# Kernel optimization log

Measured on AMD Instinct MI355X. Metric: run time of the kernel, lower is better.

## Reference

```python
import jax, jax.numpy as jnp
import numpy as np
from jax import lax

# Model dims (mamba_ssm defaults: d_state=16, d_conv=4, expand=2, dt_rank=ceil(d_model/16))
V = 16384       # vocab_size
D = 1024        # embedding_dim / d_model
C_CLS = 128     # num_CLS_classes
D_INNER = 2 * D # expand * d_model = 2048
N = 16          # d_state
K = 4           # d_conv
DT_RANK = (D + 15) // 16  # 64
B, L = 4, 512


def setup_inputs() -> dict:
    key = jax.random.key(0)
    ks = jax.random.split(key, 12)
    s = 0.02
    tokens = jax.random.randint(ks[0], (B, L), 0, V, dtype=jnp.int64)
    embedding = jax.random.normal(ks[1], (V, D), jnp.float32) * s
    in_proj_w = jax.random.normal(ks[2], (2 * D_INNER, D), jnp.float32) * s
    conv_w = jax.random.normal(ks[3], (D_INNER, 1, K), jnp.float32) * 0.1
    conv_b = jnp.zeros((D_INNER,), jnp.float32)
    x_proj_w = jax.random.normal(ks[4], (DT_RANK + 2 * N, D_INNER), jnp.float32) * s
    dt_proj_w = jax.random.normal(ks[5], (D_INNER, DT_RANK), jnp.float32) * s
    dt_proj_b = jax.random.uniform(ks[6], (D_INNER,), jnp.float32, -4.0, -2.0)  # softplus -> small dt
    A_log = jnp.log(jnp.broadcast_to(jnp.arange(1, N + 1, dtype=jnp.float32), (D_INNER, N)))
    D_param = jnp.ones((D_INNER,), jnp.float32)
    out_proj_w = jax.random.normal(ks[7], (D, D_INNER), jnp.float32) * s
    recon_w = jax.random.normal(ks[8], (V, D), jnp.float32) * s
    cls_w = jax.random.normal(ks[9], (C_CLS, D), jnp.float32) * s
    return dict(tokens=tokens, embedding=embedding, in_proj_w=in_proj_w,
                conv_w=conv_w, conv_b=conv_b, x_proj_w=x_proj_w,
                dt_proj_w=dt_proj_w, dt_proj_b=dt_proj_b, A_log=A_log,
                D_param=D_param, out_proj_w=out_proj_w, recon_w=recon_w, cls_w=cls_w)


def _mamba(h, in_proj_w, conv_w, conv_b, x_proj_w, dt_proj_w, dt_proj_b, A_log, D_param, out_proj_w):
    # h: (B, L, D)
    xz = jnp.einsum('bld,ed->ble', h, in_proj_w)          # (B, L, 2*D_INNER)
    x, z = jnp.split(xz, 2, axis=-1)                      # each (B, L, D_INNER)
    # causal depthwise conv1d along L
    xt = jnp.swapaxes(x, 1, 2)                            # (B, D_INNER, L)
    xt = lax.conv_general_dilated(xt, conv_w, window_strides=(1,),
                                  padding=[(K - 1, 0)],
                                  feature_group_count=D_INNER,
                                  dimension_numbers=('NCH', 'OIH', 'NCH'))
    xt = xt + conv_b[None, :, None]
    x = jax.nn.silu(jnp.swapaxes(xt, 1, 2))               # (B, L, D_INNER)
    # input-dependent dt, B, C
    x_dbl = jnp.einsum('bld,ed->ble', x, x_proj_w)        # (B, L, DT_RANK+2N)
    dt, Bm, Cm = jnp.split(x_dbl, [DT_RANK, DT_RANK + N], axis=-1)
    delta = jax.nn.softplus(jnp.einsum('blr,dr->bld', dt, dt_proj_w) + dt_proj_b)  # (B,L,D_INNER)
    A = -jnp.exp(A_log)                                   # (D_INNER, N)
    dA = jnp.exp(delta[..., None] * A)                    # (B,L,D_INNER,N)
    dBx = delta[..., None] * Bm[:, :, None, :] * x[..., None]  # (B,L,D_INNER,N)
    # selective scan over time (sequential recurrence)
    dA_t = jnp.swapaxes(dA, 0, 1)                         # (L,B,D_INNER,N)
    dBx_t = jnp.swapaxes(dBx, 0, 1)
    C_t = jnp.swapaxes(Cm, 0, 1)                          # (L,B,N)
    def step(hc, inp):
        a, bx, c = inp
        hc = a * hc + bx                                  # (B,D_INNER,N)
        y = jnp.einsum('bdn,bn->bd', hc, c)
        return hc, y
    h0 = jnp.zeros((x.shape[0], D_INNER, N), x.dtype)
    _, ys = lax.scan(step, h0, (dA_t, dBx_t, C_t))
    y = jnp.swapaxes(ys, 0, 1) + x * D_param              # (B,L,D_INNER)
    y = y * jax.nn.silu(z)
    return jnp.einsum('ble,de->bld', y, out_proj_w)       # (B,L,D)


def reference(tokens, embedding, in_proj_w, conv_w, conv_b, x_proj_w,
              dt_proj_w, dt_proj_b, A_log, D_param, out_proj_w, recon_w, cls_w):
    h = embedding[tokens]                                 # (B,L,D)
    h = _mamba(h, in_proj_w, conv_w, conv_b, x_proj_w, dt_proj_w, dt_proj_b,
               A_log, D_param, out_proj_w)
    recon = jnp.einsum('bld,vd->blv', h, recon_w)         # (B,L,V)
    pooled = h.mean(axis=1)                               # mean CLS pooling assumption
    cls = jnp.einsum('bd,cd->bc', pooled, cls_w)          # (B,C_CLS)
    return (recon, cls)
```

## Files before the change

### kernel.cpp

```cpp
#include <hip/hip_runtime.h>
#include <hip/hip_bf16.h>
#include <stdint.h>

#define DIN    2048
#define MROWS  2048
#define LSEQ   512
#define NV     16384
#define DMODEL 1024
#define NC     8
#define CL     64

typedef __attribute__((ext_vector_type(8))) short bf16x8;
typedef __attribute__((ext_vector_type(4))) float f32x4;

__device__ __forceinline__ uint16_t f2bf(float f) {
  uint32_t u = __builtin_bit_cast(uint32_t, f);
  u += 0x7fffu + ((u >> 16) & 1u);
  return (uint16_t)(u >> 16);
}
__device__ __forceinline__ float bf2f(uint16_t u) {
  return __builtin_bit_cast(float, (uint32_t)u << 16);
}

__device__ __forceinline__ void gld_lds16(const uint16_t* g, uint16_t* l) {
  __builtin_amdgcn_global_load_lds(
      (const __attribute__((address_space(1))) void*)g,
      (__attribute__((address_space(3))) void*)l,
      16, 0, 0);
}

__global__ __launch_bounds__(512, 2) void gemm256_bf16_kernel(
    const uint16_t* __restrict__ A, const uint16_t* __restrict__ B,
    float* __restrict__ C, int M, int N, int K)
{
  __shared__ uint16_t lds[4 * 16384];
  const int tid = threadIdx.x;
  const int w   = tid >> 6;
  const int l   = tid & 63;

  const int nwg = gridDim.x;
  const int cpx = nwg >> 3;
  const int swz = (blockIdx.x & 7) * cpx + (blockIdx.x >> 3);
  const int nmy = M >> 8;
  const int bm  = (swz % nmy) << 8;
  const int bn  = (swz / nmy) << 8;

  const int fr = l & 15;
  const int fg = l >> 4;
  const int wr = w >> 2;
  const int wc = w & 3;

  const int srow = l >> 2;
  const int kof  = (((l & 3) ^ ((l >> 3) & 3)) << 3);
  const int ar0  = (w * 2 + 0) * 16 + srow;
  const int ar1  = (w * 2 + 1) * 16 + srow;
  const uint16_t* Ag0 = A + (size_t)(bm + ar0) * K + kof;
  const uint16_t* Ag1 = A + (size_t)(bm + ar1) * K + kof;
  const uint16_t* Bg0 = B + (size_t)(bn + ar0) * K + kof;
  const uint16_t* Bg1 = B + (size_t)(bn + ar1) * K + kof;
  const int lA0 = (w * 2 + 0) * 512;
  const int lA1 = (w * 2 + 1) * 512;
  const int lB0 = 8192 + (w * 2 + 0) * 512;
  const int lB1 = 8192 + (w * 2 + 1) * 512;

  const int axr  = ((fg ^ ((fr >> 1) & 3)) << 3);
  const int aoff = (wr * 128 + fr) * 32 + axr;
  const int boff = 8192 + (wc * 64 + fr) * 32 + axr;

  f32x4 acc[8][4] = {};
  const int NT = K >> 5;

  auto stage = [&](int t) {
    const int sb = (t & 3) << 14;
    const int k0 = t << 5;
    gld_lds16(Ag0 + k0, lds + sb + lA0);
    gld_lds16(Ag1 + k0, lds + sb + lA1);
    gld_lds16(Bg0 + k0, lds + sb + lB0);
    gld_lds16(Bg1 + k0, lds + sb + lB1);
  };
  auto compute_tile = [&](int sb) {
    bf16x8 af[8], bfr[4];
#pragma unroll
    for (int mi = 0; mi < 8; ++mi)
      af[mi] = *(const bf16x8*)(lds + sb + aoff + mi * 512);
#pragma unroll
    for (int ni = 0; ni < 4; ++ni)
      bfr[ni] = *(const bf16x8*)(lds + sb + boff + ni * 512);
    __builtin_amdgcn_s_setprio(1);
#pragma unroll
    for (int mi = 0; mi < 8; ++mi)
#pragma unroll
      for (int ni = 0; ni < 4; ++ni)
        acc[mi][ni] = __builtin_amdgcn_mfma_f32_16x16x32_bf16(af[mi], bfr[ni], acc[mi][ni], 0, 0, 0);
    __builtin_amdgcn_s_setprio(0);
  };

  stage(0); stage(1); stage(2);
  asm volatile("s_waitcnt vmcnt(8)" ::: "memory");
  __builtin_amdgcn_s_barrier();

  for (int t = 0; t < NT - 3; ++t) {
    stage(t + 3);
    compute_tile((t & 3) << 14);
    asm volatile("s_waitcnt vmcnt(8)" ::: "memory");
    __builtin_amdgcn_s_barrier();
  }
  compute_tile(((NT - 3) & 3) << 14);
  asm volatile("s_waitcnt vmcnt(4)" ::: "memory");
  __builtin_amdgcn_s_barrier();
  compute_tile(((NT - 2) & 3) << 14);
  asm volatile("s_waitcnt vmcnt(0)" ::: "memory");
  __builtin_amdgcn_s_barrier();
  compute_tile(((NT - 1) & 3) << 14);

#pragma unroll
  for (int mi = 0; mi < 8; ++mi) {
    const int r0 = bm + wr * 128 + mi * 16 + fg * 4;
#pragma unroll
    for (int ni = 0; ni < 4; ++ni) {
      const int c0 = bn + wc * 64 + ni * 16 + fr;
#pragma unroll
      for (int r = 0; r < 4; ++r)
        C[(size_t)(r0 + r) * N + c0] = acc[mi][ni][r];
    }
  }
}

__global__ __launch_bounds__(256) void gemm_bf16_kernel(
    const uint16_t* __restrict__ A, const uint16_t* __restrict__ B,
    float* __restrict__ C, int M, int N, int K, int kchunk,
    const float* __restrict__ bias)
{
  __shared__ uint16_t As[128 * 32];
  __shared__ uint16_t Bs[128 * 32];
  const int tid  = threadIdx.x;
  const int wid  = tid >> 6;
  const int lane = tid & 63;
  const int bm = blockIdx.y * 128;
  const int bn = blockIdx.x * 128;
  const int k_beg = blockIdx.z * kchunk;
  float* Cout = C + (size_t)blockIdx.z * M * N;

  const int fr = lane & 15;
  const int fg = lane >> 4;
  const int wm = (wid >> 1) * 64;
  const int wn = (wid & 1) * 64;

  const int srow = wid * 32 + (lane >> 2);
  const int skof = (((lane & 3) ^ ((lane >> 2) & 3)) << 3);
  const uint16_t* Ag = A + (size_t)(bm + srow) * K + skof;
  const uint16_t* Bg = B + (size_t)(bn + srow) * K + skof;
  uint16_t* Al = As + wid * 1024;
  uint16_t* Bl = Bs + wid * 1024;

  const int cxr = ((fg ^ (fr & 3)) << 3);

  f32x4 acc[4][4] = {};

  for (int k0 = 0; k0 < kchunk; k0 += 32) {
    const int kk = k_beg + k0;
    gld_lds16(Ag + kk, Al);
    gld_lds16(Ag + (size_t)16 * K + kk, Al + 512);
    gld_lds16(Bg + kk, Bl);
    gld_lds16(Bg + (size_t)16 * K + kk, Bl + 512);
    asm volatile("s_waitcnt vmcnt(0)" ::: "memory");
    __syncthreads();
    bf16x8 af[4], bfr[4];
#pragma unroll
    for (int i = 0; i < 4; ++i)
      af[i] = *(const bf16x8*)(As + (wm + i * 16 + fr) * 32 + cxr);
#pragma unroll
    for (int j = 0; j < 4; ++j)
      bfr[j] = *(const bf16x8*)(Bs + (wn + j * 16 + fr) * 32 + cxr);
#pragma unroll
    for (int i = 0; i < 4; ++i)
#pragma unroll
      for (int j = 0; j < 4; ++j)
        acc[i][j] = __builtin_amdgcn_mfma_f32_16x16x32_bf16(af[i], bfr[j], acc[i][j], 0, 0, 0);
    __syncthreads();
  }

#pragma unroll
  for (int i = 0; i < 4; ++i) {
    const int r0 = bm + wm + i * 16 + fg * 4;
#pragma unroll
    for (int j = 0; j < 4; ++j) {
      const int c0 = bn + wn + j * 16 + fr;
      const float bv = bias ? bias[c0] : 0.f;
#pragma unroll
      for (int r = 0; r < 4; ++r) {
        float v = acc[i][j][r];
        if (bias) {
          const float u = v + bv;
          v = (u > 20.f) ? u : log1pf(__expf(u));
        }
        Cout[(size_t)(r0 + r) * N + c0] = v;
      }
    }
  }
}

__global__ __launch_bounds__(256) void reduce8_dt_kernel(
    const float* __restrict__ in, float* __restrict__ xdbl, uint16_t* __restrict__ dtb) {
  const int i = blockIdx.x * 256 + threadIdx.x;
  float s = 0.f;
#pragma unroll
  for (int z = 0; z < 8; ++z) s += in[i + (size_t)z * 262144];
  xdbl[i] = s;
  const int c = i & 127;
  if (c < 64) dtb[(i >> 7) * 64 + c] = f2bf(s);
}

__global__ __launch_bounds__(256) void reduce2_bf16_kernel(
    const float* __restrict__ in, uint16_t* __restrict__ outb, int n) {
  const int i = blockIdx.x * 256 + threadIdx.x;
  if (i >= n) return;
  outb[i] = f2bf(in[i] + in[i + (size_t)n]);
}

__global__ __launch_bounds__(256) void embed_kernel(
    const int* __restrict__ tok, const float* __restrict__ emb, uint16_t* __restrict__ out) {
  const int m = blockIdx.x;
  const int t = tok[m];
  const float4 v = ((const float4*)(emb + (size_t)t * DMODEL))[threadIdx.x];
  ((ushort4*)(out + (size_t)m * DMODEL))[threadIdx.x] =
      make_ushort4(f2bf(v.x), f2bf(v.y), f2bf(v.z), f2bf(v.w));
}

__global__ __launch_bounds__(256) void cvt_bf16_kernel(
    const float* __restrict__ in, uint16_t* __restrict__ out, int n4) {
  const int i = blockIdx.x * 256 + threadIdx.x;
  if (i >= n4) return;
  const float4 v = ((const float4*)in)[i];
  ((ushort4*)out)[i] = make_ushort4(f2bf(v.x), f2bf(v.y), f2bf(v.z), f2bf(v.w));
}

__global__ __launch_bounds__(256) void cvt_pad_kernel(
    const float* __restrict__ in, uint16_t* __restrict__ out, int rows_in, int cols4) {
  const int i = blockIdx.x * 256 + threadIdx.x;
  const int r = i / cols4, c = i % cols4;
  ushort4 o = make_ushort4(0, 0, 0, 0);
  if (r < rows_in) {
    const float4 v = ((const float4*)in)[(size_t)r * cols4 + c];
    o = make_ushort4(f2bf(v.x), f2bf(v.y), f2bf(v.z), f2bf(v.w));
  }
  ((ushort4*)out)[i] = o;
}

__global__ __launch_bounds__(256) void conv_silu_kernel(
    const float* __restrict__ xz, const float* __restrict__ cw, const float* __restrict__ cb,
    float* __restrict__ xc, uint16_t* __restrict__ xcb)
{
  const int idx = blockIdx.x * 256 + threadIdx.x;
  const int d = idx & (DIN - 1);
  const int m = idx >> 11;
  const int l = m & (LSEQ - 1);
  float acc = cb[d];
#pragma unroll
  for (int j = 0; j < 4; ++j) {
    const int lj = l - 3 + j;
    if (lj >= 0) acc += cw[d * 4 + j] * xz[(size_t)(m - 3 + j) * 4096 + d];
  }
  const float r = acc / (1.f + __expf(-acc));
  xc[idx] = r;
  xcb[idx] = f2bf(r);
}

__global__ __launch_bounds__(256) void scan_partial_kernel(
    const float* __restrict__ delta, const float* __restrict__ xc,
    const float* __restrict__ xdbl, const float* __restrict__ A_log,
    float* __restrict__ Pb, float* __restrict__ Qb)
{
  const int q = threadIdx.x & 3;
  const int d_idx = threadIdx.x >> 2;
  const int c = blockIdx.x;
  const int d = blockIdx.y * 64 + d_idx;
  const int b = blockIdx.z;
  float Arow[4];
#pragma unroll
  for (int n = 0; n < 4; ++n)
    Arow[n] = -expf(A_log[d * 16 + q * 4 + n]);
  float P[4] = {1.f, 1.f, 1.f, 1.f};
  float Q[4] = {0.f, 0.f, 0.f, 0.f};
  const int l0 = c * CL;
#pragma unroll 4
  for (int li = 0; li < CL; ++li) {
    const int m = b * LSEQ + l0 + li;
    const float de = delta[(size_t)m * DIN + d];
    const float xv = xc[(size_t)m * DIN + d];
    const float dx = de * xv;
    const float4 Bv = *(const float4*)(xdbl + (size_t)m * 128 + 64 + q * 4);
    const float bv[4] = {Bv.x, Bv.y, Bv.z, Bv.w};
#pragma unroll
    for (int n = 0; n < 4; ++n) {
      const float a = __expf(de * Arow[n]);
      P[n] *= a;
      Q[n] = a * Q[n] + dx * bv[n];
    }
  }
  const size_t o = ((size_t)(b * NC + c) * DIN + d) * 16 + q * 4;
  *(float4*)(Pb + o) = make_float4(P[0], P[1], P[2], P[3]);
  *(float4*)(Qb + o) = make_float4(Q[0], Q[1], Q[2], Q[3]);
}

__global__ __launch_bounds__(256) void scan_bounds_kernel(
    const float* __restrict__ Pb, const float* __restrict__ Qb, float* __restrict__ Hi)
{
  const int i = blockIdx.x * 256 + threadIdx.x;
  const int b = i >> 15;
  const int r = i & 32767;
  float h = 0.f;
#pragma unroll
  for (int c = 0; c < NC; ++c) {
    const size_t o = ((size_t)(b * NC + c) << 15) + r;
    Hi[o] = h;
    h = Pb[o] * h + Qb[o];
  }
}

__global__ __launch_bounds__(256) void scan_final_kernel(
    const float* __restrict__ delta, const float* __restrict__ xc,
    const float* __restrict__ xdbl, const float* __restrict__ xz,
    const float* __restrict__ A_log, const float* __restrict__ Dp,
    const float* __restrict__ Hi, uint16_t* __restrict__ yb)
{
  const int q = threadIdx.x & 3;
  const int d_idx = threadIdx.x >> 2;
  const int c = blockIdx.x;
  const int d = blockIdx.y * 64 + d_idx;
  const int b = blockIdx.z;
  float Arow[4];
#pragma unroll
  for (int n = 0; n < 4; ++n)
    Arow[n] = -expf(A_log[d * 16 + q * 4 + n]);
  const float dpd = Dp[d];
  const size_t o = ((size_t)(b * NC + c) * DIN + d) * 16 + q * 4;
  const float4 Hv = *(const float4*)(Hi + o);
  float h[4] = {Hv.x, Hv.y, Hv.z, Hv.w};
  const int l0 = c * CL;
#pragma unroll 2
  for (int li = 0; li < CL; ++li) {
    const int m = b * LSEQ + l0 + li;
    const float de = delta[(size_t)m * DIN + d];
    const float xv = xc[(size_t)m * DIN + d];
    const float dx = de * xv;
    const float4 Bv = *(const float4*)(xdbl + (size_t)m * 128 + 64 + q * 4);
    const float4 Cv = *(const float4*)(xdbl + (size_t)m * 128 + 80 + q * 4);
    const float bv[4] = {Bv.x, Bv.y, Bv.z, Bv.w};
    const float cv[4] = {Cv.x, Cv.y, Cv.z, Cv.w};
    float yp = 0.f;
#pragma unroll
    for (int n = 0; n < 4; ++n) {
      const float a = __expf(de * Arow[n]);
      h[n] = a * h[n] + dx * bv[n];
      yp += h[n] * cv[n];
    }
    yp += __shfl_xor(yp, 1);
    yp += __shfl_xor(yp, 2);
    if (q == 0) {
      const float z = xz[(size_t)m * 4096 + 2048 + d];
      const float sil = z / (1.f + __expf(-z));
      yb[(size_t)m * DIN + d] = f2bf((yp + xv * dpd) * sil);
    }
  }
}

__global__ __launch_bounds__(256) void pool1_kernel(
    const uint16_t* __restrict__ h2b, float* __restrict__ part) {
  const int b = blockIdx.x >> 4, s = blockIdx.x & 15;
  const int c = threadIdx.x * 4;
  const uint16_t* base = h2b + ((size_t)(b * LSEQ + s * 32)) * DMODEL + c;
  float a0 = 0, a1 = 0, a2 = 0, a3 = 0;
  for (int l = 0; l < 32; ++l) {
    const ushort4 v = *(const ushort4*)(base + (size_t)l * DMODEL);
    a0 += bf2f(v.x); a1 += bf2f(v.y); a2 += bf2f(v.z); a3 += bf2f(v.w);
  }
  *(float4*)(part + (size_t)blockIdx.x * DMODEL + c) = make_float4(a0, a1, a2, a3);
}

__global__ __launch_bounds__(256) void pool2_cls_kernel(
    const float* __restrict__ part, const float* __restrict__ w, float* __restrict__ out) {
  __shared__ float pl[DMODEL];
  const int b = blockIdx.x, t = threadIdx.x;
  float4 s = make_float4(0, 0, 0, 0);
  for (int k = 0; k < 16; ++k) {
    const float4 v = *(const float4*)(part + ((size_t)(b * 16 + k)) * DMODEL + t * 4);
    s.x += v.x; s.y += v.y; s.z += v.z; s.w += v.w;
  }
  const float inv = 1.f / (float)LSEQ;
  pl[t * 4 + 0] = s.x * inv; pl[t * 4 + 1] = s.y * inv;
  pl[t * 4 + 2] = s.z * inv; pl[t * 4 + 3] = s.w * inv;
  __syncthreads();
  if (t < 128) {
    const float* wr = w + (size_t)t * DMODEL;
    float acc = 0.f;
    for (int k = 0; k < DMODEL; ++k) acc += pl[k] * wr[k];
    out[b * 128 + t] = acc;
  }
}

extern "C" void kernel_launch(void* const* d_in, const int* in_sizes, int n_in,
                              void* d_out, int out_size, void* d_ws, size_t ws_size,
                              hipStream_t stream) {
  const int*   tokens    = (const int*)d_in[0];
  const float* embedding = (const float*)d_in[1];
  const float* in_proj_w = (const float*)d_in[2];
  const float* conv_w    = (const float*)d_in[3];
  const float* conv_b    = (const float*)d_in[4];
  const float* x_proj_w  = (const float*)d_in[5];
  const float* dt_proj_w = (const float*)d_in[6];
  const float* dt_proj_b = (const float*)d_in[7];
  const float* A_log     = (const float*)d_in[8];
  const float* D_param   = (const float*)d_in[9];
  const float* out_prj_w = (const float*)d_in[10];
  const float* recon_w   = (const float*)d_in[11];
  const float* cls_w     = (const float*)d_in[12];

  char* ws = (char*)d_ws;
  const size_t MB = 1024 * 1024;
  uint16_t* h_bf   = (uint16_t*)(ws + 0);
  uint16_t* w_in   = (uint16_t*)(ws + 4 * MB);
  float*    xz     = (float*)(ws + 12 * MB);
  float*    xc_f   = (float*)(ws + 44 * MB);
  uint16_t* xc_b   = (uint16_t*)(ws + 60 * MB);
  uint16_t* wx_bf  = (uint16_t*)(ws + 68 * MB);
  float*    xdbl   = (float*)(ws + 69 * MB);
  uint16_t* dt_bf  = (uint16_t*)(ws + 70 * MB);
  uint16_t* wdt_bf = (uint16_t*)(ws + 71 * MB);
  float*    delta  = (float*)(ws + 72 * MB);
  uint16_t* y_bf   = (uint16_t*)(ws + 88 * MB);
  uint16_t* h2_bf  = (uint16_t*)(ws + 96 * MB);
  float*    part   = (float*)(ws + 100 * MB);
  uint16_t* wout_bf = h_bf;
  uint16_t* wrec_bf = (uint16_t*)xz;
  float*    kscr    = delta;
  float*    Pbuf    = (float*)(ws + 60 * MB);
  float*    Qbuf    = (float*)(ws + 64 * MB);
  float*    Hinit   = (float*)(ws + 4 * MB);

  const int RECON = MROWS * NV;

  embed_kernel<<<dim3(MROWS), dim3(256), 0, stream>>>(tokens, embedding, h_bf);
  cvt_bf16_kernel<<<dim3(4096), dim3(256), 0, stream>>>(in_proj_w, w_in, 4096 * 1024 / 4);
  gemm_bf16_kernel<<<dim3(32, 16, 1), dim3(256), 0, stream>>>(h_bf, w_in, xz, MROWS, 4096, 1024, 1024, nullptr);
  cvt_bf16_kernel<<<dim3(2048), dim3(256), 0, stream>>>(out_prj_w, wout_bf, 1024 * 2048 / 4);
  cvt_bf16_kernel<<<dim3(128), dim3(256), 0, stream>>>(dt_proj_w, wdt_bf, 2048 * 64 / 4);
  cvt_pad_kernel<<<dim3(256), dim3(256), 0, stream>>>(x_proj_w, wx_bf, 96, 512);
  conv_silu_kernel<<<dim3(16384), dim3(256), 0, stream>>>(xz, conv_w, conv_b, xc_f, xc_b);
  gemm_bf16_kernel<<<dim3(1, 16, 8), dim3(256), 0, stream>>>(xc_b, wx_bf, kscr, MROWS, 128, 2048, 256, nullptr);
  reduce8_dt_kernel<<<dim3(1024), dim3(256), 0, stream>>>(kscr, xdbl, dt_bf);
  gemm_bf16_kernel<<<dim3(16, 16, 1), dim3(256), 0, stream>>>(dt_bf, wdt_bf, delta, MROWS, DIN, 64, 64, dt_proj_b);
  scan_partial_kernel<<<dim3(NC, 32, 4), dim3(256), 0, stream>>>(delta, xc_f, xdbl, A_log, Pbuf, Qbuf);
  scan_bounds_kernel<<<dim3(512), dim3(256), 0, stream>>>(Pbuf, Qbuf, Hinit);
  scan_final_kernel<<<dim3(NC, 32, 4), dim3(256), 0, stream>>>(delta, xc_f, xdbl, xz, A_log, D_param, Hinit, y_bf);
  cvt_bf16_kernel<<<dim3(16384), dim3(256), 0, stream>>>(recon_w, wrec_bf, NV * 1024 / 4);
  gemm_bf16_kernel<<<dim3(8, 16, 2), dim3(256), 0, stream>>>(y_bf, wout_bf, kscr, MROWS, 1024, 2048, 1024, nullptr);
  reduce2_bf16_kernel<<<dim3(8192), dim3(256), 0, stream>>>(kscr, h2_bf, MROWS * 1024);
  gemm256_bf16_kernel<<<dim3(512), dim3(512), 0, stream>>>(h2_bf, wrec_bf, (float*)d_out, MROWS, NV, 1024);
  pool1_kernel<<<dim3(64), dim3(256), 0, stream>>>(h2_bf, part);
  pool2_cls_kernel<<<dim3(4), dim3(256), 0, stream>>>(part, cls_w, (float*)d_out + RECON);
}
```

Before: 363.3 us.

## Store xz and conv output in bf16, vectorize conv, merge weight conversions

The in_proj GEMM now writes bf16 directly, and the conv/SiLU kernel reads bf16 four channels at a time and only emits a bf16 output. The scan kernels read xc and z from bf16 buffers. Three small weight-conversion launches are merged into one, and the workspace is relaid out with the out_proj GEMM moved before the recon weight conversion. This reduces memory traffic for the large intermediates at the cost of extra bf16 rounding in the scan inputs.

```diff
diff --git a/kernel.cpp b/kernel.cpp
--- a/kernel.cpp
+++ b/kernel.cpp
@@ -128,8 +128,8 @@
 
 __global__ __launch_bounds__(256) void gemm_bf16_kernel(
     const uint16_t* __restrict__ A, const uint16_t* __restrict__ B,
-    float* __restrict__ C, int M, int N, int K, int kchunk,
-    const float* __restrict__ bias)
+    float* __restrict__ Cf, uint16_t* __restrict__ Cbf,
+    int M, int N, int K, int kchunk, const float* __restrict__ bias)
 {
   __shared__ uint16_t As[128 * 32];
   __shared__ uint16_t Bs[128 * 32];
@@ -139,7 +139,7 @@
   const int bm = blockIdx.y * 128;
   const int bn = blockIdx.x * 128;
   const int k_beg = blockIdx.z * kchunk;
-  float* Cout = C + (size_t)blockIdx.z * M * N;
+  float* Cout = Cf + (size_t)blockIdx.z * M * N;
 
   const int fr = lane & 15;
   const int fg = lane >> 4;
@@ -194,9 +194,35 @@
           const float u = v + bv;
           v = (u > 20.f) ? u : log1pf(__expf(u));
         }
-        Cout[(size_t)(r0 + r) * N + c0] = v;
+        if (Cbf) Cbf[(size_t)(r0 + r) * N + c0] = f2bf(v);
+        else     Cout[(size_t)(r0 + r) * N + c0] = v;
       }
     }
+  }
+}
+
+__global__ __launch_bounds__(256) void cvt_weights_kernel(
+    const float* __restrict__ wo, const float* __restrict__ wdt, const float* __restrict__ wx,
+    uint16_t* __restrict__ wob, uint16_t* __restrict__ wdtb, uint16_t* __restrict__ wxb)
+{
+  const int bid = blockIdx.x;
+  if (bid < 2048) {
+    const int i = bid * 256 + threadIdx.x;
+    const float4 v = ((const float4*)wo)[i];
+    ((ushort4*)wob)[i] = make_ushort4(f2bf(v.x), f2bf(v.y), f2bf(v.z), f2bf(v.w));
+  } else if (bid < 2176) {
+    const int i = (bid - 2048) * 256 + threadIdx.x;
+    const float4 v = ((const float4*)wdt)[i];
+    ((ushort4*)wdtb)[i] = make_ushort4(f2bf(v.x), f2bf(v.y), f2bf(v.z), f2bf(v.w));
+  } else {
+    const int i = (bid - 2176) * 256 + threadIdx.x;
+    const int r = i >> 9, c = i & 511;
+    ushort4 o = make_ushort4(0, 0, 0, 0);
+    if (r < 96) {
+      const float4 v = ((const float4*)wx)[(size_t)r * 512 + c];
+      o = make_ushort4(f2bf(v.x), f2bf(v.y), f2bf(v.z), f2bf(v.w));
+    }
+    ((ushort4*)wxb)[i] = o;
   }
 }
 
@@ -235,39 +261,45 @@
   ((ushort4*)out)[i] = make_ushort4(f2bf(v.x), f2bf(v.y), f2bf(v.z), f2bf(v.w));
 }
 
-__global__ __launch_bounds__(256) void cvt_pad_kernel(
-    const float* __restrict__ in, uint16_t* __restrict__ out, int rows_in, int cols4) {
-  const int i = blockIdx.x * 256 + threadIdx.x;
-  const int r = i / cols4, c = i % cols4;
-  ushort4 o = make_ushort4(0, 0, 0, 0);
-  if (r < rows_in) {
-    const float4 v = ((const float4*)in)[(size_t)r * cols4 + c];
-    o = make_ushort4(f2bf(v.x), f2bf(v.y), f2bf(v.z), f2bf(v.w));
-  }
-  ((ushort4*)out)[i] = o;
-}
-
 __global__ __launch_bounds__(256) void conv_silu_kernel(
-    const float* __restrict__ xz, const float* __restrict__ cw, const float* __restrict__ cb,
-    float* __restrict__ xc, uint16_t* __restrict__ xcb)
+    const uint16_t* __restrict__ xzb, const float* __restrict__ cw, const float* __restrict__ cb,
+    uint16_t* __restrict__ xcb)
 {
   const int idx = blockIdx.x * 256 + threadIdx.x;
-  const int d = idx & (DIN - 1);
-  const int m = idx >> 11;
-  const int l = m & (LSEQ - 1);
-  float acc = cb[d];
+  const int d4  = idx & 511;
+  const int m   = idx >> 9;
+  const int l   = m & (LSEQ - 1);
+  const int d   = d4 << 2;
+  const float4 cbv = *(const float4*)(cb + d);
+  float a0 = cbv.x, a1 = cbv.y, a2 = cbv.z, a3 = cbv.w;
+  const float4 w0 = *(const float4*)(cw + (d + 0) * 4);
+  const float4 w1 = *(const float4*)(cw + (d + 1) * 4);
+  const float4 w2 = *(const float4*)(cw + (d + 2) * 4);
+  const float4 w3 = *(const float4*)(cw + (d + 3) * 4);
+  const float wj0[4] = {w0.x, w0.y, w0.z, w0.w};
+  const float wj1[4] = {w1.x, w1.y, w1.z, w1.w};
+  const float wj2[4] = {w2.x, w2.y, w2.z, w2.w};
+  const float wj3[4] = {w3.x, w3.y, w3.z, w3.w};
 #pragma unroll
   for (int j = 0; j < 4; ++j) {
     const int lj = l - 3 + j;
-    if (lj >= 0) acc += cw[d * 4 + j] * xz[(size_t)(m - 3 + j) * 4096 + d];
-  }
-  const float r = acc / (1.f + __expf(-acc));
-  xc[idx] = r;
-  xcb[idx] = f2bf(r);
+    if (lj >= 0) {
+      const ushort4 x = *(const ushort4*)(xzb + (size_t)(m - 3 + j) * 4096 + d);
+      a0 += wj0[j] * bf2f(x.x);
+      a1 += wj1[j] * bf2f(x.y);
+      a2 += wj2[j] * bf2f(x.z);
+      a3 += wj3[j] * bf2f(x.w);
+    }
+  }
+  const float r0 = a0 / (1.f + __expf(-a0));
+  const float r1 = a1 / (1.f + __expf(-a1));
+  const float r2 = a2 / (1.f + __expf(-a2));
+  const float r3 = a3 / (1.f + __expf(-a3));
+  *(ushort4*)(xcb + (size_t)m * DIN + d) = make_ushort4(f2bf(r0), f2bf(r1), f2bf(r2), f2bf(r3));
 }
 
 __global__ __launch_bounds__(256) void scan_partial_kernel(
-    const float* __restrict__ delta, const float* __restrict__ xc,
+    const float* __restrict__ delta, const uint16_t* __restrict__ xcb,
     const float* __restrict__ xdbl, const float* __restrict__ A_log,
     float* __restrict__ Pb, float* __restrict__ Qb)
 {
@@ -287,7 +319,7 @@
   for (int li = 0; li < CL; ++li) {
     const int m = b * LSEQ + l0 + li;
     const float de = delta[(size_t)m * DIN + d];
-    const float xv = xc[(size_t)m * DIN + d];
+    const float xv = bf2f(xcb[(size_t)m * DIN + d]);
     const float dx = de * xv;
     const float4 Bv = *(const float4*)(xdbl + (size_t)m * 128 + 64 + q * 4);
     const float bv[4] = {Bv.x, Bv.y, Bv.z, Bv.w};
@@ -319,8 +351,8 @@
 }
 
 __global__ __launch_bounds__(256) void scan_final_kernel(
-    const float* __restrict__ delta, const float* __restrict__ xc,
-    const float* __restrict__ xdbl, const float* __restrict__ xz,
+    const float* __restrict__ delta, const uint16_t* __restrict__ xcb,
+    const float* __restrict__ xdbl, const uint16_t* __restrict__ xzb,
     const float* __restrict__ A_log, const float* __restrict__ Dp,
     const float* __restrict__ Hi, uint16_t* __restrict__ yb)
 {
@@ -342,7 +374,7 @@
   for (int li = 0; li < CL; ++li) {
     const int m = b * LSEQ + l0 + li;
     const float de = delta[(size_t)m * DIN + d];
-    const float xv = xc[(size_t)m * DIN + d];
+    const float xv = bf2f(xcb[(size_t)m * DIN + d]);
     const float dx = de * xv;
     const float4 Bv = *(const float4*)(xdbl + (size_t)m * 128 + 64 + q * 4);
     const float4 Cv = *(const float4*)(xdbl + (size_t)m * 128 + 80 + q * 4);
@@ -358,7 +390,7 @@
     yp += __shfl_xor(yp, 1);
     yp += __shfl_xor(yp, 2);
     if (q == 0) {
-      const float z = xz[(size_t)m * 4096 + 2048 + d];
+      const float z = bf2f(xzb[(size_t)m * 4096 + 2048 + d]);
       const float sil = z / (1.f + __expf(-z));
       yb[(size_t)m * DIN + d] = f2bf((yp + xv * dpd) * sil);
     }
@@ -420,42 +452,39 @@
   const size_t MB = 1024 * 1024;
   uint16_t* h_bf   = (uint16_t*)(ws + 0);
   uint16_t* w_in   = (uint16_t*)(ws + 4 * MB);
-  float*    xz     = (float*)(ws + 12 * MB);
-  float*    xc_f   = (float*)(ws + 44 * MB);
-  uint16_t* xc_b   = (uint16_t*)(ws + 60 * MB);
-  uint16_t* wx_bf  = (uint16_t*)(ws + 68 * MB);
-  float*    xdbl   = (float*)(ws + 69 * MB);
-  uint16_t* dt_bf  = (uint16_t*)(ws + 70 * MB);
-  uint16_t* wdt_bf = (uint16_t*)(ws + 71 * MB);
-  float*    delta  = (float*)(ws + 72 * MB);
-  uint16_t* y_bf   = (uint16_t*)(ws + 88 * MB);
-  uint16_t* h2_bf  = (uint16_t*)(ws + 96 * MB);
-  float*    part   = (float*)(ws + 100 * MB);
+  uint16_t* xz_bf  = (uint16_t*)(ws + 12 * MB);
+  uint16_t* xc_b   = (uint16_t*)(ws + 28 * MB);
+  uint16_t* wx_bf  = (uint16_t*)(ws + 36 * MB);
+  uint16_t* dt_bf  = (uint16_t*)(ws + 36 * MB + 512 * 1024);
+  uint16_t* wdt_bf = (uint16_t*)(ws + 36 * MB + 768 * 1024);
+  float*    xdbl   = (float*)(ws + 37 * MB);
+  float*    delta  = (float*)(ws + 38 * MB);
+  float*    Pbuf   = (float*)(ws + 54 * MB);
+  float*    Qbuf   = (float*)(ws + 58 * MB);
+  uint16_t* y_bf   = (uint16_t*)(ws + 62 * MB);
+  uint16_t* h2_bf  = (uint16_t*)(ws + 70 * MB);
+  float*    part   = (float*)(ws + 74 * MB);
   uint16_t* wout_bf = h_bf;
-  uint16_t* wrec_bf = (uint16_t*)xz;
+  float*    Hinit   = (float*)(ws + 4 * MB);
   float*    kscr    = delta;
-  float*    Pbuf    = (float*)(ws + 60 * MB);
-  float*    Qbuf    = (float*)(ws + 64 * MB);
-  float*    Hinit   = (float*)(ws + 4 * MB);
+  uint16_t* wrec_bf = (uint16_t*)(ws + 38 * MB);
 
   const int RECON = MROWS * NV;
 
   embed_kernel<<<dim3(MROWS), dim3(256), 0, stream>>>(tokens, embedding, h_bf);
   cvt_bf16_kernel<<<dim3(4096), dim3(256), 0, stream>>>(in_proj_w, w_in, 4096 * 1024 / 4);
-  gemm_bf16_kernel<<<dim3(32, 16, 1), dim3(256), 0, stream>>>(h_bf, w_in, xz, MROWS, 4096, 1024, 1024, nullptr);
-  cvt_bf16_kernel<<<dim3(2048), dim3(256), 0, stream>>>(out_prj_w, wout_bf, 1024 * 2048 / 4);
-  cvt_bf16_kernel<<<dim3(128), dim3(256), 0, stream>>>(dt_proj_w, wdt_bf, 2048 * 64 / 4);
-  cvt_pad_kernel<<<dim3(256), dim3(256), 0, stream>>>(x_proj_w, wx_bf, 96, 512);
-  conv_silu_kernel<<<dim3(16384), dim3(256), 0, stream>>>(xz, conv_w, conv_b, xc_f, xc_b);
-  gemm_bf16_kernel<<<dim3(1, 16, 8), dim3(256), 0, stream>>>(xc_b, wx_bf, kscr, MROWS, 128, 2048, 256, nullptr);
+  gemm_bf16_kernel<<<dim3(32, 16, 1), dim3(256), 0, stream>>>(h_bf, w_in, nullptr, xz_bf, MROWS, 4096, 1024, 1024, nullptr);
+  cvt_weights_kernel<<<dim3(2432), dim3(256), 0, stream>>>(out_prj_w, dt_proj_w, x_proj_w, wout_bf, wdt_bf, wx_bf);
+  conv_silu_kernel<<<dim3(4096), dim3(256), 0, stream>>>(xz_bf, conv_w, conv_b, xc_b);
+  gemm_bf16_kernel<<<dim3(1, 16, 8), dim3(256), 0, stream>>>(xc_b, wx_bf, kscr, nullptr, MROWS, 128, 2048, 256, nullptr);
   reduce8_dt_kernel<<<dim3(1024), dim3(256), 0, stream>>>(kscr, xdbl, dt_bf);
-  gemm_bf16_kernel<<<dim3(16, 16, 1), dim3(256), 0, stream>>>(dt_bf, wdt_bf, delta, MROWS, DIN, 64, 64, dt_proj_b);
-  scan_partial_kernel<<<dim3(NC, 32, 4), dim3(256), 0, stream>>>(delta, xc_f, xdbl, A_log, Pbuf, Qbuf);
+  gemm_bf16_kernel<<<dim3(16, 16, 1), dim3(256), 0, stream>>>(dt_bf, wdt_bf, delta, nullptr, MROWS, DIN, 64, 64, dt_proj_b);
+  scan_partial_kernel<<<dim3(NC, 32, 4), dim3(256), 0, stream>>>(delta, xc_b, xdbl, A_log, Pbuf, Qbuf);
   scan_bounds_kernel<<<dim3(512), dim3(256), 0, stream>>>(Pbuf, Qbuf, Hinit);
-  scan_final_kernel<<<dim3(NC, 32, 4), dim3(256), 0, stream>>>(delta, xc_f, xdbl, xz, A_log, D_param, Hinit, y_bf);
+  scan_final_kernel<<<dim3(NC, 32, 4), dim3(256), 0, stream>>>(delta, xc_b, xdbl, xz_bf, A_log, D_param, Hinit, y_bf);
+  gemm_bf16_kernel<<<dim3(8, 16, 2), dim3(256), 0, stream>>>(y_bf, wout_bf, kscr, nullptr, MROWS, 1024, 2048, 1024, nullptr);
+  reduce2_bf16_kernel<<<dim3(8192), dim3(256), 0, stream>>>(kscr, h2_bf, MROWS * 1024);
   cvt_bf16_kernel<<<dim3(16384), dim3(256), 0, stream>>>(recon_w, wrec_bf, NV * 1024 / 4);
-  gemm_bf16_kernel<<<dim3(8, 16, 2), dim3(256), 0, stream>>>(y_bf, wout_bf, kscr, MROWS, 1024, 2048, 1024, nullptr);
-  reduce2_bf16_kernel<<<dim3(8192), dim3(256), 0, stream>>>(kscr, h2_bf, MROWS * 1024);
   gemm256_bf16_kernel<<<dim3(512), dim3(512), 0, stream>>>(h2_bf, wrec_bf, (float*)d_out, MROWS, NV, 1024);
   pool1_kernel<<<dim3(64), dim3(256), 0, stream>>>(h2_bf, part);
   pool2_cls_kernel<<<dim3(4), dim3(256), 0, stream>>>(part, cls_w, (float*)d_out + RECON);
```

New measurement: 359.2 us. About the same (-1.1%).
